# Optimization experiments

Hardware: AMD Instinct MI355X
Metric: run time of the kernel (lower is better)

The kernel has to match this reference:

```python
import jax, jax.numpy as jnp
import numpy as np

B, S, H = 2, 4096, 256
NH, NKV = 8, 4
HD = H // NH          # 32
GROUPS = NH // NKV    # 2
ROPE_BASE = 10000.0


def _rope_cos_sin(seq_len, dim, dtype):
    inv_freq = 1.0 / (ROPE_BASE ** (jnp.arange(0, dim, 2, dtype=jnp.float32) / dim))
    t = jnp.arange(seq_len, dtype=jnp.float32)
    freqs = jnp.outer(t, inv_freq)            # [S, dim/2]
    emb = jnp.concatenate([freqs, freqs], -1)  # [S, dim]
    return jnp.cos(emb).astype(dtype), jnp.sin(emb).astype(dtype)


def _rotate_half(x):
    x1, x2 = jnp.split(x, 2, axis=-1)
    return jnp.concatenate([-x2, x1], axis=-1)


def setup_inputs() -> dict:
    key = jax.random.key(0)
    k0, k1, k2, k3, k4 = jax.random.split(key, 5)
    return {
        "hidden_states": jax.random.normal(k0, (B, S, H), jnp.float32),
        "Wq": jax.random.normal(k1, (H, H), jnp.float32) * 0.02,
        "Wk": jax.random.normal(k2, (NKV * HD, H), jnp.float32) * 0.02,
        "Wv": jax.random.normal(k3, (NKV * HD, H), jnp.float32) * 0.02,
        "Wo": jax.random.normal(k4, (H, H), jnp.float32) * 0.02,
    }


def reference(hidden_states, Wq, Wk, Wv, Wo):
    b, s, _ = hidden_states.shape
    # projections (nn.Linear: x @ W.T)
    q = (hidden_states @ Wq.T).reshape(b, s, NH, HD).transpose(0, 2, 1, 3)   # [b,nh,s,hd]
    k = (hidden_states @ Wk.T).reshape(b, s, NKV, HD).transpose(0, 2, 1, 3)  # [b,nkv,s,hd]
    v = (hidden_states @ Wv.T).reshape(b, s, NKV, HD).transpose(0, 2, 1, 3)
    # RoPE
    cos, sin = _rope_cos_sin(s, HD, hidden_states.dtype)  # [s,hd]
    q = q * cos + _rotate_half(q) * sin
    k = k * cos + _rotate_half(k) * sin
    # GQA: repeat kv heads (repeat_interleave over head dim)
    k = jnp.repeat(k, GROUPS, axis=1)  # [b,nh,s,hd]
    v = jnp.repeat(v, GROUPS, axis=1)
    # scores + causal mask
    scores = jnp.einsum('bhqd,bhkd->bhqk', q, k) / jnp.sqrt(jnp.float32(HD)).astype(q.dtype)
    causal = jnp.triu(jnp.full((s, s), -jnp.inf, dtype=scores.dtype), k=1)
    scores = scores + causal
    attn = jax.nn.softmax(scores.astype(jnp.float32), axis=-1).astype(q.dtype)
    out = jnp.einsum('bhqk,bhkd->bhqd', attn, v)          # [b,nh,s,hd]
    out = out.transpose(0, 2, 1, 3).reshape(b, s, NH * HD)
    return out @ Wo.T
```

## Files before the change

kernel.cpp:

```cpp
#include <hip/hip_runtime.h>
#include <hip/hip_bf16.h>
#include <stdint.h>

#define NB 2
#define SEQ 4096
#define HID 256
#define NHEAD 8
#define NKVH 4
#define HDIM 32

typedef __bf16 bf16;
typedef __bf16 bf16x8 __attribute__((ext_vector_type(8)));
typedef float f32x4 __attribute__((ext_vector_type(4)));

static __device__ __forceinline__ uint16_t bfbits(float f) {
    bf16 h = (bf16)f;
    return __builtin_bit_cast(uint16_t, h);
}
static __device__ __forceinline__ uint32_t pack_bf16(float lo, float hi) {
    return (uint32_t)bfbits(lo) | ((uint32_t)bfbits(hi) << 16);
}
static __device__ __forceinline__ float fexp2(float x) {
#if __has_builtin(__builtin_amdgcn_exp2f)
    return __builtin_amdgcn_exp2f(x);
#else
    float r; asm("v_exp_f32 %0, %1" : "=v"(r) : "v"(x)); return r;
#endif
}
static __device__ __forceinline__ void gld_lds16(const void* g, void* l) {
    __builtin_amdgcn_global_load_lds(
        (const __attribute__((address_space(1))) void*)g,
        (__attribute__((address_space(3))) void*)l, 16, 0, 0);
}

__global__ __launch_bounds__(256) void to_bf16(
    const float* __restrict__ hs, const float* __restrict__ Wq,
    const float* __restrict__ Wk, const float* __restrict__ Wv,
    const float* __restrict__ Wo,
    bf16* __restrict__ hsb, bf16* __restrict__ Wb, bf16* __restrict__ Wob)
{
    size_t idx = ((size_t)blockIdx.x * 256 + threadIdx.x) * 8;
    const float* src; bf16* dst; size_t off;
    if (idx < 2097152)      { src = hs; dst = hsb;        off = idx; }
    else if (idx < 2162688) { src = Wq; dst = Wb;         off = idx - 2097152; }
    else if (idx < 2195456) { src = Wk; dst = Wb + 65536; off = idx - 2162688; }
    else if (idx < 2228224) { src = Wv; dst = Wb + 98304; off = idx - 2195456; }
    else                    { src = Wo; dst = Wob;        off = idx - 2228224; }
    float4 a = *(const float4*)&src[off];
    float4 b = *(const float4*)&src[off + 4];
    uint32_t u0 = pack_bf16(a.x, a.y);
    uint32_t u1 = pack_bf16(a.z, a.w);
    uint32_t u2 = pack_bf16(b.x, b.y);
    uint32_t u3 = pack_bf16(b.z, b.w);
    *(uint4*)&dst[off] = make_uint4(u0, u1, u2, u3);
}

__global__ __launch_bounds__(256, 2) void qkv2(
    const bf16* __restrict__ hsb, const bf16* __restrict__ Wb,
    bf16* __restrict__ qws, bf16* __restrict__ kws, bf16* __restrict__ vtws)
{
    __shared__ bf16 As[64 * 256];
    __shared__ bf16 Bs[64 * 256];
    const int t = threadIdx.x;
    const int wid = t >> 6, lane = t & 63;
    const int g = lane >> 4, c = lane & 15;
    const int n0 = blockIdx.x * 64;
    const int m0 = blockIdx.y * 64;

    {
        const int half = lane >> 5;
        const int seg = lane & 31;
        #pragma unroll
        for (int i = 0; i < 8; ++i) {
            const int row = (i * 4 + wid) * 2 + half;
            const int sseg = seg ^ (row & 7);
            gld_lds16(hsb + (size_t)(m0 + row) * 256 + sseg * 8,
                      (char*)As + wid * 1024 + i * 4096);
            gld_lds16(Wb + (size_t)(n0 + row) * 256 + sseg * 8,
                      (char*)Bs + wid * 1024 + i * 4096);
        }
    }
    __syncthreads();

    const f32x4 zf = {0.f, 0.f, 0.f, 0.f};
    f32x4 acc[4] = {zf, zf, zf, zf};
    const int r = wid * 16 + c;
    const int aBase = r * 512;
    const int s7 = c & 7;
    #pragma unroll
    for (int j = 0; j < 8; ++j) {
        const int so = ((4 * j + g) ^ s7) << 4;
        bf16x8 af = *(const bf16x8*)((const char*)As + aBase + so);
        #pragma unroll
        for (int nt = 0; nt < 4; ++nt) {
            bf16x8 bfr = *(const bf16x8*)((const char*)Bs + (nt * 16 + c) * 512 + so);
            acc[nt] = __builtin_amdgcn_mfma_f32_16x16x32_bf16(af, bfr, acc[nt], 0, 0, 0);
        }
    }

    const float qscale = 1.4426950408889634f * 0.17677669529663687f;
    const float invf = exp2f(-0.83048202372184f * (float)c);
    #pragma unroll
    for (int rr = 0; rr < 4; ++rr) {
        int m = m0 + wid * 16 + g * 4 + rr;
        int b = m >> 12, s = m & (SEQ - 1);
        float sn, cs;
        sincosf((float)s * invf, &sn, &cs);
        if (n0 < 256) {
            #pragma unroll
            for (int np = 0; np < 4; np += 2) {
                int h = (n0 + np * 16) >> 5;
                float x1 = acc[np][rr], x2 = acc[np + 1][rr];
                float y1 = (x1 * cs - x2 * sn) * qscale;
                float y2 = (x2 * cs + x1 * sn) * qscale;
                size_t base = ((size_t)(b * NHEAD + h) * SEQ + s) * HDIM;
                qws[base + c] = (bf16)y1;
                qws[base + 16 + c] = (bf16)y2;
            }
        } else if (n0 < 384) {
            #pragma unroll
            for (int np = 0; np < 4; np += 2) {
                int kh = (n0 - 256 + np * 16) >> 5;
                float x1 = acc[np][rr], x2 = acc[np + 1][rr];
                float y1 = x1 * cs - x2 * sn;
                float y2 = x2 * cs + x1 * sn;
                size_t base = ((size_t)(b * NKVH + kh) * SEQ + s) * HDIM;
                kws[base + c] = (bf16)y1;
                kws[base + 16 + c] = (bf16)y2;
            }
        } else {
            #pragma unroll
            for (int nt = 0; nt < 4; ++nt) {
                int ng = n0 + nt * 16 + c - 384;
                int vh = ng >> 5, d = ng & 31;
                vtws[((size_t)(b * NKVH + vh) * HDIM + d) * SEQ + s] = (bf16)acc[nt][rr];
            }
        }
    }
}

#define ATT_CHUNK(CI, KBUF, VBUF)                                              \
  do {                                                                         \
    const char* kbuf = (KBUF);                                                 \
    const char* vbuf = (VBUF);                                                 \
    bf16x8 kf0 = *(const bf16x8*)(kbuf + kro);                                 \
    bf16x8 kf1 = *(const bf16x8*)(kbuf + kro + 256);                           \
    bf16x8 kf2 = *(const bf16x8*)(kbuf + kro + 2048);                          \
    bf16x8 kf3 = *(const bf16x8*)(kbuf + kro + 2304);                          \
    bf16x8 vf00 = *(const bf16x8*)(vbuf + vro0 + ((g ^ cx) << 4));             \
    bf16x8 vf01 = *(const bf16x8*)(vbuf + vro1 + ((g ^ cx) << 4));             \
    bf16x8 vf10 = *(const bf16x8*)(vbuf + vro0 + (((4 + g) ^ cx) << 4));       \
    bf16x8 vf11 = *(const bf16x8*)(vbuf + vro1 + (((4 + g) ^ cx) << 4));       \
    const bool diag = ((CI) == d_w);                                           \
    const int qbase = (w & 1) * 32 + c;                                        \
    {                                                                          \
        f32x4 st0 = __builtin_amdgcn_mfma_f32_16x16x32_bf16(kf0, qf0, zf, 0, 0, 0); \
        f32x4 st1 = __builtin_amdgcn_mfma_f32_16x16x32_bf16(kf1, qf0, zf, 0, 0, 0); \
        f32x4 st2 = __builtin_amdgcn_mfma_f32_16x16x32_bf16(kf2, qf0, zf, 0, 0, 0); \
        f32x4 st3 = __builtin_amdgcn_mfma_f32_16x16x32_bf16(kf3, qf0, zf, 0, 0, 0); \
        if (diag) {                                                            \
            const int qoff = qbase;                                            \
            _Pragma("unroll")                                                  \
            for (int rr = 0; rr < 4; ++rr) {                                   \
                if (8 * g + rr > qoff)          st0[rr] = -1e30f;              \
                if (8 * g + 4 + rr > qoff)      st1[rr] = -1e30f;              \
                if (32 + 8 * g + rr > qoff)     st2[rr] = -1e30f;              \
                if (32 + 8 * g + 4 + rr > qoff) st3[rr] = -1e30f;              \
            }                                                                  \
        }                                                                      \
        float p00 = fexp2(st0[0]), p01 = fexp2(st0[1]), p02 = fexp2(st0[2]), p03 = fexp2(st0[3]); \
        float p10 = fexp2(st1[0]), p11 = fexp2(st1[1]), p12 = fexp2(st1[2]), p13 = fexp2(st1[3]); \
        float p20 = fexp2(st2[0]), p21 = fexp2(st2[1]), p22 = fexp2(st2[2]), p23 = fexp2(st2[3]); \
        float p30 = fexp2(st3[0]), p31 = fexp2(st3[1]), p32 = fexp2(st3[2]), p33 = fexp2(st3[3]); \
        union { uint32_t u[4]; bf16x8 v; } pb0, pb1;                           \
        asm("v_cvt_pk_bf16_f32 %0, %1, %2" : "=v"(pb0.u[0]) : "v"(p00), "v"(p01)); \
        asm("v_cvt_pk_bf16_f32 %0, %1, %2" : "=v"(pb0.u[1]) : "v"(p02), "v"(p03)); \
        asm("v_cvt_pk_bf16_f32 %0, %1, %2" : "=v"(pb0.u[2]) : "v"(p10), "v"(p11)); \
        asm("v_cvt_pk_bf16_f32 %0, %1, %2" : "=v"(pb0.u[3]) : "v"(p12), "v"(p13)); \
        asm("v_cvt_pk_bf16_f32 %0, %1, %2" : "=v"(pb1.u[0]) : "v"(p20), "v"(p21)); \
        asm("v_cvt_pk_bf16_f32 %0, %1, %2" : "=v"(pb1.u[1]) : "v"(p22), "v"(p23)); \
        asm("v_cvt_pk_bf16_f32 %0, %1, %2" : "=v"(pb1.u[2]) : "v"(p30), "v"(p31)); \
        asm("v_cvt_pk_bf16_f32 %0, %1, %2" : "=v"(pb1.u[3]) : "v"(p32), "v"(p33)); \
        o00 = __builtin_amdgcn_mfma_f32_16x16x32_bf16(vf00, pb0.v, o00, 0, 0, 0); \
        o01 = __builtin_amdgcn_mfma_f32_16x16x32_bf16(vf01, pb0.v, o01, 0, 0, 0); \
        ol0 = __builtin_amdgcn_mfma_f32_16x16x32_bf16(onesf.v, pb0.v, ol0, 0, 0, 0); \
        o00 = __builtin_amdgcn_mfma_f32_16x16x32_bf16(vf10, pb1.v, o00, 0, 0, 0); \
        o01 = __builtin_amdgcn_mfma_f32_16x16x32_bf16(vf11, pb1.v, o01, 0, 0, 0); \
        ol0 = __builtin_amdgcn_mfma_f32_16x16x32_bf16(onesf.v, pb1.v, ol0, 0, 0, 0); \
    }                                                                          \
    {                                                                          \
        f32x4 st0 = __builtin_amdgcn_mfma_f32_16x16x32_bf16(kf0, qf1, zf, 0, 0, 0); \
        f32x4 st1 = __builtin_amdgcn_mfma_f32_16x16x32_bf16(kf1, qf1, zf, 0, 0, 0); \
        f32x4 st2 = __builtin_amdgcn_mfma_f32_16x16x32_bf16(kf2, qf1, zf, 0, 0, 0); \
        f32x4 st3 = __builtin_amdgcn_mfma_f32_16x16x32_bf16(kf3, qf1, zf, 0, 0, 0); \
        if (diag) {                                                            \
            const int qoff = qbase + 16;                                       \
            _Pragma("unroll")                                                  \
            for (int rr = 0; rr < 4; ++rr) {                                   \
                if (8 * g + rr > qoff)          st0[rr] = -1e30f;              \
                if (8 * g + 4 + rr > qoff)      st1[rr] = -1e30f;              \
                if (32 + 8 * g + rr > qoff)     st2[rr] = -1e30f;              \
                if (32 + 8 * g + 4 + rr > qoff) st3[rr] = -1e30f;              \
            }                                                                  \
        }                                                                      \
        float p00 = fexp2(st0[0]), p01 = fexp2(st0[1]), p02 = fexp2(st0[2]), p03 = fexp2(st0[3]); \
        float p10 = fexp2(st1[0]), p11 = fexp2(st1[1]), p12 = fexp2(st1[2]), p13 = fexp2(st1[3]); \
        float p20 = fexp2(st2[0]), p21 = fexp2(st2[1]), p22 = fexp2(st2[2]), p23 = fexp2(st2[3]); \
        float p30 = fexp2(st3[0]), p31 = fexp2(st3[1]), p32 = fexp2(st3[2]), p33 = fexp2(st3[3]); \
        union { uint32_t u[4]; bf16x8 v; } pb0, pb1;                           \
        asm("v_cvt_pk_bf16_f32 %0, %1, %2" : "=v"(pb0.u[0]) : "v"(p00), "v"(p01)); \
        asm("v_cvt_pk_bf16_f32 %0, %1, %2" : "=v"(pb0.u[1]) : "v"(p02), "v"(p03)); \
        asm("v_cvt_pk_bf16_f32 %0, %1, %2" : "=v"(pb0.u[2]) : "v"(p10), "v"(p11)); \
        asm("v_cvt_pk_bf16_f32 %0, %1, %2" : "=v"(pb0.u[3]) : "v"(p12), "v"(p13)); \
        asm("v_cvt_pk_bf16_f32 %0, %1, %2" : "=v"(pb1.u[0]) : "v"(p20), "v"(p21)); \
        asm("v_cvt_pk_bf16_f32 %0, %1, %2" : "=v"(pb1.u[1]) : "v"(p22), "v"(p23)); \
        asm("v_cvt_pk_bf16_f32 %0, %1, %2" : "=v"(pb1.u[2]) : "v"(p30), "v"(p31)); \
        asm("v_cvt_pk_bf16_f32 %0, %1, %2" : "=v"(pb1.u[3]) : "v"(p32), "v"(p33)); \
        o10 = __builtin_amdgcn_mfma_f32_16x16x32_bf16(vf00, pb0.v, o10, 0, 0, 0); \
        o11 = __builtin_amdgcn_mfma_f32_16x16x32_bf16(vf01, pb0.v, o11, 0, 0, 0); \
        ol1 = __builtin_amdgcn_mfma_f32_16x16x32_bf16(onesf.v, pb0.v, ol1, 0, 0, 0); \
        o10 = __builtin_amdgcn_mfma_f32_16x16x32_bf16(vf10, pb1.v, o10, 0, 0, 0); \
        o11 = __builtin_amdgcn_mfma_f32_16x16x32_bf16(vf11, pb1.v, o11, 0, 0, 0); \
        ol1 = __builtin_amdgcn_mfma_f32_16x16x32_bf16(onesf.v, pb1.v, ol1, 0, 0, 0); \
    }                                                                          \
  } while (0)

__global__ __launch_bounds__(256, 4) void attn_fwd(
    const bf16* __restrict__ qws, const bf16* __restrict__ kws,
    const bf16* __restrict__ vtws,
    float* __restrict__ Oa, float* __restrict__ Ob,
    float* __restrict__ la, float* __restrict__ lb)
{
    __shared__ char smem[32768];
    const int t = threadIdx.x;
    const int w = t >> 6, lane = t & 63;
    const int g = lane >> 4, c = lane & 15;
    const int wg = blockIdx.x;
    const int h = wg & 7;
    const int rest = wg >> 3;
    const int half = rest & 1;
    const int r2 = rest >> 1;
    const int b = r2 & 1;
    const int T = 31 - (r2 >> 1);
    const int kvh = h >> 1;
    const bf16* Kg = kws + (size_t)(b * NKVH + kvh) * SEQ * HDIM;
    const bf16* Vg = vtws + (size_t)(b * NKVH + kvh) * HDIM * SEQ;
    const int cbase = half * (T + 1);
    const int nloc = T + 1;
    const int q0 = T * 128 + w * 32;
    const int d_w = 2 * T + (w >> 1);

    const bf16* Qb = qws + (size_t)(b * NHEAD + h) * SEQ * HDIM;
    bf16x8 qf0 = *(const bf16x8*)&Qb[(size_t)(q0 + c) * HDIM + g * 8];
    bf16x8 qf1 = *(const bf16x8*)&Qb[(size_t)(q0 + 16 + c) * HDIM + g * 8];

    const int sd = t >> 3, sseg = t & 7;
    const bf16* kg_t = Kg + t * 8;
    const bf16* vg_t = Vg + (size_t)sd * SEQ + (sseg ^ (sd & 7)) * 8;
    char* kl = smem + w * 1024;
    char* vl = smem + 16384 + w * 1024;

    const int kperm = 8 * (c >> 2) + (c & 3);
    const int kro = kperm * 64 + g * 16;
    const int cx = c & 7;
    const int vro0 = c * 128, vro1 = (16 + c) * 128;

    const f32x4 zf = {0.f, 0.f, 0.f, 0.f};
    union { uint32_t u[4]; bf16x8 v; } onesf;
    onesf.u[0] = onesf.u[1] = onesf.u[2] = onesf.u[3] = 0x3F803F80u;

    f32x4 o00 = zf, o01 = zf, ol0 = zf;
    f32x4 o10 = zf, o11 = zf, ol1 = zf;

    gld_lds16(kg_t + (size_t)cbase * 2048, kl);
    gld_lds16(vg_t + (size_t)cbase * 64, vl);
    if (1 < nloc) {
        gld_lds16(kg_t + (size_t)(cbase + 1) * 2048, kl + 4096);
        gld_lds16(vg_t + (size_t)(cbase + 1) * 64, vl + 4096);
    }
    __syncthreads();

    const int nit = (nloc + 1) >> 1;
    #pragma unroll 1
    for (int it = 0; it < nit; ++it) {
        const int s0 = 2 * it, s1 = s0 + 1;
        if (s0 + 2 < nloc) {
            gld_lds16(kg_t + (size_t)(cbase + s0 + 2) * 2048, kl + ((s0 + 2) & 3) * 4096);
            gld_lds16(vg_t + (size_t)(cbase + s0 + 2) * 64, vl + ((s0 + 2) & 3) * 4096);
        }
        if (s1 + 2 < nloc) {
            gld_lds16(kg_t + (size_t)(cbase + s1 + 2) * 2048, kl + ((s1 + 2) & 3) * 4096);
            gld_lds16(vg_t + (size_t)(cbase + s1 + 2) * 64, vl + ((s1 + 2) & 3) * 4096);
        }
        const int ci0 = cbase + s0;
        if (ci0 <= d_w) {
            ATT_CHUNK(ci0, smem + (s0 & 3) * 4096 + 0,
                           smem + 16384 + (s0 & 3) * 4096);
        }
        const int ci1 = cbase + s1;
        if (s1 < nloc && ci1 <= d_w) {
            ATT_CHUNK(ci1, smem + (s1 & 3) * 4096 + 0,
                           smem + 16384 + (s1 & 3) * 4096);
        }
        __syncthreads();
    }

    float* tr = (float*)(smem + w * 2112);
    float* Op = half ? Ob : Oa;
    float* lp = half ? lb : la;
    #pragma unroll 1
    for (int j = 0; j < 2; ++j) {
        f32x4 a0 = j ? o10 : o00;
        f32x4 a1 = j ? o11 : o01;
        f32x4 al = j ? ol1 : ol0;
        #pragma unroll
        for (int rr = 0; rr < 4; ++rr) {
            tr[c * 33 + 4 * g + rr]      = a0[rr];
            tr[c * 33 + 16 + 4 * g + rr] = a1[rr];
        }
        if (g == 0) lp[((size_t)b * SEQ + q0 + j * 16 + c) * 8 + h] = al[0];
        int q = lane >> 2, dp = (lane & 3) * 8;
        size_t m = (size_t)b * SEQ + q0 + j * 16 + q;
        float4 f0 = make_float4(tr[q * 33 + dp + 0], tr[q * 33 + dp + 1],
                                tr[q * 33 + dp + 2], tr[q * 33 + dp + 3]);
        float4 f1 = make_float4(tr[q * 33 + dp + 4], tr[q * 33 + dp + 5],
                                tr[q * 33 + dp + 6], tr[q * 33 + dp + 7]);
        *(float4*)&Op[m * HID + h * HDIM + dp]     = f0;
        *(float4*)&Op[m * HID + h * HDIM + dp + 4] = f1;
    }
}

__global__ __launch_bounds__(256) void combine(
    const float* __restrict__ Oa, const float* __restrict__ Ob,
    const float* __restrict__ la, const float* __restrict__ lb,
    bf16* __restrict__ att)
{
    const size_t e = ((size_t)blockIdx.x * 256 + threadIdx.x) * 8;
    const size_t m = e >> 8;
    const int hh = (int)(e & 255) >> 5;
    const float inv = 1.0f / (la[m * 8 + hh] + lb[m * 8 + hh]);
    float4 a0 = *(const float4*)&Oa[e];
    float4 a1 = *(const float4*)&Oa[e + 4];
    float4 b0 = *(const float4*)&Ob[e];
    float4 b1 = *(const float4*)&Ob[e + 4];
    uint32_t u0 = pack_bf16((a0.x + b0.x) * inv, (a0.y + b0.y) * inv);
    uint32_t u1 = pack_bf16((a0.z + b0.z) * inv, (a0.w + b0.w) * inv);
    uint32_t u2 = pack_bf16((a1.x + b1.x) * inv, (a1.y + b1.y) * inv);
    uint32_t u3 = pack_bf16((a1.z + b1.z) * inv, (a1.w + b1.w) * inv);
    *(uint4*)&att[e] = make_uint4(u0, u1, u2, u3);
}

__global__ __launch_bounds__(256, 2) void out_proj2(
    const bf16* __restrict__ att, const bf16* __restrict__ Wob,
    float* __restrict__ out)
{
    __shared__ bf16 As[64 * 256];
    __shared__ bf16 Bs[64 * 256];
    const int t = threadIdx.x;
    const int wid = t >> 6, lane = t & 63;
    const int g = lane >> 4, c = lane & 15;
    const int n0 = blockIdx.x * 64;
    const int m0 = blockIdx.y * 64;

    {
        const int half = lane >> 5;
        const int seg = lane & 31;
        #pragma unroll
        for (int i = 0; i < 8; ++i) {
            const int row = (i * 4 + wid) * 2 + half;
            const int sseg = seg ^ (row & 7);
            gld_lds16(att + (size_t)(m0 + row) * 256 + sseg * 8,
                      (char*)As + wid * 1024 + i * 4096);
            gld_lds16(Wob + (size_t)(n0 + row) * 256 + sseg * 8,
                      (char*)Bs + wid * 1024 + i * 4096);
        }
    }
    __syncthreads();

    const f32x4 zf = {0.f, 0.f, 0.f, 0.f};
    f32x4 acc[4] = {zf, zf, zf, zf};
    const int r = wid * 16 + c;
    const int aBase = r * 512;
    const int s7 = c & 7;
    #pragma unroll
    for (int j = 0; j < 8; ++j) {
        const int so = ((4 * j + g) ^ s7) << 4;
        bf16x8 af = *(const bf16x8*)((const char*)As + aBase + so);
        #pragma unroll
        for (int nt = 0; nt < 4; ++nt) {
            bf16x8 bfr = *(const bf16x8*)((const char*)Bs + (nt * 16 + c) * 512 + so);
            acc[nt] = __builtin_amdgcn_mfma_f32_16x16x32_bf16(af, bfr, acc[nt], 0, 0, 0);
        }
    }

    #pragma unroll
    for (int nt = 0; nt < 4; ++nt) {
        #pragma unroll
        for (int rr = 0; rr < 4; ++rr) {
            int m = m0 + wid * 16 + g * 4 + rr;
            out[(size_t)m * HID + n0 + nt * 16 + c] = acc[nt][rr];
        }
    }
}

extern "C" void kernel_launch(void* const* d_in, const int* in_sizes, int n_in,
                              void* d_out, int out_size, void* d_ws, size_t ws_size,
                              hipStream_t stream) {
    const float* hs = (const float*)d_in[0];
    const float* Wq = (const float*)d_in[1];
    const float* Wk = (const float*)d_in[2];
    const float* Wv = (const float*)d_in[3];
    const float* Wo = (const float*)d_in[4];
    char* ws = (char*)d_ws;
    bf16* qws  = (bf16*)(ws);
    bf16* kws  = (bf16*)(ws + 4194304);
    bf16* vtws = (bf16*)(ws + 6291456);
    bf16* att  = (bf16*)(ws + 8388608);
    float* Oa  = (float*)(ws + 12582912);
    float* Ob  = (float*)(ws + 20971520);
    float* la  = (float*)(ws + 29360128);
    float* lb  = (float*)(ws + 29622272);
    bf16* hsb  = (bf16*)(ws + 29884416);
    bf16* Wb   = (bf16*)(ws + 34078720);
    bf16* Wob  = (bf16*)(ws + 34340864);

    to_bf16<<<1120, 256, 0, stream>>>(hs, Wq, Wk, Wv, Wo, hsb, Wb, Wob);
    qkv2<<<dim3(8, 128), 256, 0, stream>>>(hsb, Wb, qws, kws, vtws);
    attn_fwd<<<1024, 256, 0, stream>>>(qws, kws, vtws, Oa, Ob, la, lb);
    combine<<<1024, 256, 0, stream>>>(Oa, Ob, la, lb, att);
    out_proj2<<<dim3(4, 128), 256, 0, stream>>>(att, Wob, (float*)d_out);
}
```

Measured before the change: 62.30 us.

## Fuse bf16 conversion into QKV projection and combine into output projection

Drops the separate fp32-to-bf16 conversion kernel and the split-attention combine kernel. The QKV projection now loads fp32 inputs and weights directly and converts them while staging into padded LDS in two K-chunks. The output projection does the same, merging the two partial attention outputs and normalizing them as it stages the A tile, and uses a wider 128-column N tile. This cuts two launches and the intermediate bf16 round-trips, in exchange for synchronous register-path loads instead of direct global-to-LDS loads, weights re-converted by every block, and a smaller grid for the output projection.

New measurement: 71.04 us. 14.0% more time.

```diff
diff --git a/kernel.cpp b/kernel.cpp
--- a/kernel.cpp
+++ b/kernel.cpp
@@ -33,76 +33,63 @@
         (__attribute__((address_space(3))) void*)l, 16, 0, 0);
 }
 
-__global__ __launch_bounds__(256) void to_bf16(
+__global__ __launch_bounds__(256) void qkv_proj(
     const float* __restrict__ hs, const float* __restrict__ Wq,
     const float* __restrict__ Wk, const float* __restrict__ Wv,
-    const float* __restrict__ Wo,
-    bf16* __restrict__ hsb, bf16* __restrict__ Wb, bf16* __restrict__ Wob)
-{
-    size_t idx = ((size_t)blockIdx.x * 256 + threadIdx.x) * 8;
-    const float* src; bf16* dst; size_t off;
-    if (idx < 2097152)      { src = hs; dst = hsb;        off = idx; }
-    else if (idx < 2162688) { src = Wq; dst = Wb;         off = idx - 2097152; }
-    else if (idx < 2195456) { src = Wk; dst = Wb + 65536; off = idx - 2162688; }
-    else if (idx < 2228224) { src = Wv; dst = Wb + 98304; off = idx - 2195456; }
-    else                    { src = Wo; dst = Wob;        off = idx - 2228224; }
-    float4 a = *(const float4*)&src[off];
-    float4 b = *(const float4*)&src[off + 4];
-    uint32_t u0 = pack_bf16(a.x, a.y);
-    uint32_t u1 = pack_bf16(a.z, a.w);
-    uint32_t u2 = pack_bf16(b.x, b.y);
-    uint32_t u3 = pack_bf16(b.z, b.w);
-    *(uint4*)&dst[off] = make_uint4(u0, u1, u2, u3);
-}
-
-__global__ __launch_bounds__(256, 2) void qkv2(
-    const bf16* __restrict__ hsb, const bf16* __restrict__ Wb,
     bf16* __restrict__ qws, bf16* __restrict__ kws, bf16* __restrict__ vtws)
 {
-    __shared__ bf16 As[64 * 256];
-    __shared__ bf16 Bs[64 * 256];
+    __shared__ bf16 As[64][136];
+    __shared__ bf16 Bs[64][136];
     const int t = threadIdx.x;
     const int wid = t >> 6, lane = t & 63;
     const int g = lane >> 4, c = lane & 15;
     const int n0 = blockIdx.x * 64;
     const int m0 = blockIdx.y * 64;
 
-    {
-        const int half = lane >> 5;
-        const int seg = lane & 31;
-        #pragma unroll
-        for (int i = 0; i < 8; ++i) {
-            const int row = (i * 4 + wid) * 2 + half;
-            const int sseg = seg ^ (row & 7);
-            gld_lds16(hsb + (size_t)(m0 + row) * 256 + sseg * 8,
-                      (char*)As + wid * 1024 + i * 4096);
-            gld_lds16(Wb + (size_t)(n0 + row) * 256 + sseg * 8,
-                      (char*)Bs + wid * 1024 + i * 4096);
-        }
-    }
-    __syncthreads();
+    const float* bsrc; int ro;
+    if (n0 < 256)      { bsrc = Wq; ro = n0; }
+    else if (n0 < 384) { bsrc = Wk; ro = n0 - 256; }
+    else               { bsrc = Wv; ro = n0 - 384; }
 
     const f32x4 zf = {0.f, 0.f, 0.f, 0.f};
     f32x4 acc[4] = {zf, zf, zf, zf};
-    const int r = wid * 16 + c;
-    const int aBase = r * 512;
-    const int s7 = c & 7;
-    #pragma unroll
-    for (int j = 0; j < 8; ++j) {
-        const int so = ((4 * j + g) ^ s7) << 4;
-        bf16x8 af = *(const bf16x8*)((const char*)As + aBase + so);
-        #pragma unroll
-        for (int nt = 0; nt < 4; ++nt) {
-            bf16x8 bfr = *(const bf16x8*)((const char*)Bs + (nt * 16 + c) * 512 + so);
-            acc[nt] = __builtin_amdgcn_mfma_f32_16x16x32_bf16(af, bfr, acc[nt], 0, 0, 0);
+
+    const int c4 = t & 31;
+    const int rb = t >> 5;
+
+    for (int ks = 0; ks < 256; ks += 128) {
+        __syncthreads();
+        #pragma unroll
+        for (int i = 0; i < 8; ++i) {
+            int row = i * 8 + rb;
+            float4 v = *(const float4*)&hs[(size_t)(m0 + row) * HID + ks + c4 * 4];
+            ushort4 w; w.x = bfbits(v.x); w.y = bfbits(v.y); w.z = bfbits(v.z); w.w = bfbits(v.w);
+            *(ushort4*)&As[row][c4 * 4] = w;
+        }
+        #pragma unroll
+        for (int i = 0; i < 8; ++i) {
+            int row = i * 8 + rb;
+            float4 v = *(const float4*)&bsrc[(size_t)(ro + row) * HID + ks + c4 * 4];
+            ushort4 w; w.x = bfbits(v.x); w.y = bfbits(v.y); w.z = bfbits(v.z); w.w = bfbits(v.w);
+            *(ushort4*)&Bs[row][c4 * 4] = w;
+        }
+        __syncthreads();
+        #pragma unroll
+        for (int kk = 0; kk < 128; kk += 32) {
+            bf16x8 af = *(const bf16x8*)&As[wid * 16 + c][kk + g * 8];
+            #pragma unroll
+            for (int nt = 0; nt < 4; ++nt) {
+                bf16x8 bfr = *(const bf16x8*)&Bs[nt * 16 + c][kk + g * 8];
+                acc[nt] = __builtin_amdgcn_mfma_f32_16x16x32_bf16(af, bfr, acc[nt], 0, 0, 0);
+            }
         }
     }
 
     const float qscale = 1.4426950408889634f * 0.17677669529663687f;
     const float invf = exp2f(-0.83048202372184f * (float)c);
     #pragma unroll
-    for (int rr = 0; rr < 4; ++rr) {
-        int m = m0 + wid * 16 + g * 4 + rr;
+    for (int r = 0; r < 4; ++r) {
+        int m = m0 + wid * 16 + g * 4 + r;
         int b = m >> 12, s = m & (SEQ - 1);
         float sn, cs;
         sincosf((float)s * invf, &sn, &cs);
@@ -110,7 +97,7 @@
             #pragma unroll
             for (int np = 0; np < 4; np += 2) {
                 int h = (n0 + np * 16) >> 5;
-                float x1 = acc[np][rr], x2 = acc[np + 1][rr];
+                float x1 = acc[np][r], x2 = acc[np + 1][r];
                 float y1 = (x1 * cs - x2 * sn) * qscale;
                 float y2 = (x2 * cs + x1 * sn) * qscale;
                 size_t base = ((size_t)(b * NHEAD + h) * SEQ + s) * HDIM;
@@ -121,7 +108,7 @@
             #pragma unroll
             for (int np = 0; np < 4; np += 2) {
                 int kh = (n0 - 256 + np * 16) >> 5;
-                float x1 = acc[np][rr], x2 = acc[np + 1][rr];
+                float x1 = acc[np][r], x2 = acc[np + 1][r];
                 float y1 = x1 * cs - x2 * sn;
                 float y2 = x2 * cs + x1 * sn;
                 size_t base = ((size_t)(b * NKVH + kh) * SEQ + s) * HDIM;
@@ -133,7 +120,7 @@
             for (int nt = 0; nt < 4; ++nt) {
                 int ng = n0 + nt * 16 + c - 384;
                 int vh = ng >> 5, d = ng & 31;
-                vtws[((size_t)(b * NKVH + vh) * HDIM + d) * SEQ + s] = (bf16)acc[nt][rr];
+                vtws[((size_t)(b * NKVH + vh) * HDIM + d) * SEQ + s] = (bf16)acc[nt][r];
             }
         }
     }
@@ -330,71 +317,64 @@
     }
 }
 
-__global__ __launch_bounds__(256) void combine(
+__global__ __launch_bounds__(256, 2) void outp3(
     const float* __restrict__ Oa, const float* __restrict__ Ob,
     const float* __restrict__ la, const float* __restrict__ lb,
-    bf16* __restrict__ att)
+    const float* __restrict__ Wo, float* __restrict__ out)
 {
-    const size_t e = ((size_t)blockIdx.x * 256 + threadIdx.x) * 8;
-    const size_t m = e >> 8;
-    const int hh = (int)(e & 255) >> 5;
-    const float inv = 1.0f / (la[m * 8 + hh] + lb[m * 8 + hh]);
-    float4 a0 = *(const float4*)&Oa[e];
-    float4 a1 = *(const float4*)&Oa[e + 4];
-    float4 b0 = *(const float4*)&Ob[e];
-    float4 b1 = *(const float4*)&Ob[e + 4];
-    uint32_t u0 = pack_bf16((a0.x + b0.x) * inv, (a0.y + b0.y) * inv);
-    uint32_t u1 = pack_bf16((a0.z + b0.z) * inv, (a0.w + b0.w) * inv);
-    uint32_t u2 = pack_bf16((a1.x + b1.x) * inv, (a1.y + b1.y) * inv);
-    uint32_t u3 = pack_bf16((a1.z + b1.z) * inv, (a1.w + b1.w) * inv);
-    *(uint4*)&att[e] = make_uint4(u0, u1, u2, u3);
-}
-
-__global__ __launch_bounds__(256, 2) void out_proj2(
-    const bf16* __restrict__ att, const bf16* __restrict__ Wob,
-    float* __restrict__ out)
-{
-    __shared__ bf16 As[64 * 256];
-    __shared__ bf16 Bs[64 * 256];
+    __shared__ bf16 As[64][136];
+    __shared__ bf16 Bs[128][136];
     const int t = threadIdx.x;
     const int wid = t >> 6, lane = t & 63;
     const int g = lane >> 4, c = lane & 15;
-    const int n0 = blockIdx.x * 64;
+    const int n0 = blockIdx.x * 128;
     const int m0 = blockIdx.y * 64;
 
-    {
-        const int half = lane >> 5;
-        const int seg = lane & 31;
+    const int c4 = t & 31;
+    const int rb = t >> 5;
+
+    const f32x4 zf = {0.f, 0.f, 0.f, 0.f};
+    f32x4 acc[8] = {zf, zf, zf, zf, zf, zf, zf, zf};
+
+    for (int ks = 0; ks < 256; ks += 128) {
+        __syncthreads();
+        const int col = ks + c4 * 4;
+        const int hh = col >> 5;
         #pragma unroll
         for (int i = 0; i < 8; ++i) {
-            const int row = (i * 4 + wid) * 2 + half;
-            const int sseg = seg ^ (row & 7);
-            gld_lds16(att + (size_t)(m0 + row) * 256 + sseg * 8,
-                      (char*)As + wid * 1024 + i * 4096);
-            gld_lds16(Wob + (size_t)(n0 + row) * 256 + sseg * 8,
-                      (char*)Bs + wid * 1024 + i * 4096);
-        }
-    }
-    __syncthreads();
-
-    const f32x4 zf = {0.f, 0.f, 0.f, 0.f};
-    f32x4 acc[4] = {zf, zf, zf, zf};
-    const int r = wid * 16 + c;
-    const int aBase = r * 512;
-    const int s7 = c & 7;
+            const int row = i * 8 + rb;
+            const size_t m = (size_t)(m0 + row);
+            const float inv = 1.0f / (la[m * 8 + hh] + lb[m * 8 + hh]);
+            float4 a = *(const float4*)&Oa[m * HID + col];
+            float4 b = *(const float4*)&Ob[m * HID + col];
+            ushort4 w;
+            w.x = bfbits((a.x + b.x) * inv);
+            w.y = bfbits((a.y + b.y) * inv);
+            w.z = bfbits((a.z + b.z) * inv);
+            w.w = bfbits((a.w + b.w) * inv);
+            *(ushort4*)&As[row][c4 * 4] = w;
+        }
+        #pragma unroll
+        for (int i = 0; i < 16; ++i) {
+            const int row = i * 8 + rb;
+            float4 v = *(const float4*)&Wo[(size_t)(n0 + row) * HID + col];
+            ushort4 w; w.x = bfbits(v.x); w.y = bfbits(v.y); w.z = bfbits(v.z); w.w = bfbits(v.w);
+            *(ushort4*)&Bs[row][c4 * 4] = w;
+        }
+        __syncthreads();
+        #pragma unroll
+        for (int kk = 0; kk < 128; kk += 32) {
+            bf16x8 af = *(const bf16x8*)&As[wid * 16 + c][kk + g * 8];
+            #pragma unroll
+            for (int nt = 0; nt < 8; ++nt) {
+                bf16x8 bfr = *(const bf16x8*)&Bs[nt * 16 + c][kk + g * 8];
+                acc[nt] = __builtin_amdgcn_mfma_f32_16x16x32_bf16(af, bfr, acc[nt], 0, 0, 0);
+            }
+        }
+    }
+
     #pragma unroll
-    for (int j = 0; j < 8; ++j) {
-        const int so = ((4 * j + g) ^ s7) << 4;
-        bf16x8 af = *(const bf16x8*)((const char*)As + aBase + so);
-        #pragma unroll
-        for (int nt = 0; nt < 4; ++nt) {
-            bf16x8 bfr = *(const bf16x8*)((const char*)Bs + (nt * 16 + c) * 512 + so);
-            acc[nt] = __builtin_amdgcn_mfma_f32_16x16x32_bf16(af, bfr, acc[nt], 0, 0, 0);
-        }
-    }
-
-    #pragma unroll
-    for (int nt = 0; nt < 4; ++nt) {
+    for (int nt = 0; nt < 8; ++nt) {
         #pragma unroll
         for (int rr = 0; rr < 4; ++rr) {
             int m = m0 + wid * 16 + g * 4 + rr;
@@ -415,18 +395,12 @@
     bf16* qws  = (bf16*)(ws);
     bf16* kws  = (bf16*)(ws + 4194304);
     bf16* vtws = (bf16*)(ws + 6291456);
-    bf16* att  = (bf16*)(ws + 8388608);
-    float* Oa  = (float*)(ws + 12582912);
-    float* Ob  = (float*)(ws + 20971520);
-    float* la  = (float*)(ws + 29360128);
-    float* lb  = (float*)(ws + 29622272);
-    bf16* hsb  = (bf16*)(ws + 29884416);
-    bf16* Wb   = (bf16*)(ws + 34078720);
-    bf16* Wob  = (bf16*)(ws + 34340864);
-
-    to_bf16<<<1120, 256, 0, stream>>>(hs, Wq, Wk, Wv, Wo, hsb, Wb, Wob);
-    qkv2<<<dim3(8, 128), 256, 0, stream>>>(hsb, Wb, qws, kws, vtws);
+    float* Oa  = (float*)(ws + 8388608);
+    float* Ob  = (float*)(ws + 16777216);
+    float* la  = (float*)(ws + 25165824);
+    float* lb  = (float*)(ws + 25427968);
+
+    qkv_proj<<<dim3(8, 128), 256, 0, stream>>>(hs, Wq, Wk, Wv, qws, kws, vtws);
     attn_fwd<<<1024, 256, 0, stream>>>(qws, kws, vtws, Oa, Ob, la, lb);
-    combine<<<1024, 256, 0, stream>>>(Oa, Ob, la, lb, att);
-    out_proj2<<<dim3(4, 128), 256, 0, stream>>>(att, Wob, (float*)d_out);
-}
+    outp3<<<dim3(2, 128), 256, 0, stream>>>(Oa, Ob, la, lb, Wo, (float*)d_out);
+}
```
